# Performance work log

Hardware: AMD Instinct MI355X
Metric: run time of the kernel (lower is better)

Reference implementation:

```python
import jax, jax.numpy as jnp
import numpy as np

DIM = 512
DEPTH = 4
E = 2 ** DEPTH          # 16 experts
HID = 4 * DIM           # mult = 4
B, S = 8, 4096


def setup_inputs() -> dict:
    key = jax.random.key(0)
    ks = jax.random.split(key, 7)
    sc_in = 1.0 / np.sqrt(DIM)
    sc_hid = 1.0 / np.sqrt(HID)
    return {
        "x": jax.random.normal(ks[0], (B, S, DIM), jnp.float32),
        "Wr": jax.random.normal(ks[1], (E - 1, DIM), jnp.float32) * sc_in,
        "br": jax.random.normal(ks[2], (E - 1,), jnp.float32) * 0.01,
        "W1": jax.random.normal(ks[3], (E, DIM, HID), jnp.float32) * sc_in,
        "b1": jax.random.normal(ks[4], (E, HID), jnp.float32) * 0.01,
        "W2": jax.random.normal(ks[5], (E, HID, DIM), jnp.float32) * sc_hid,
        "b2": jax.random.normal(ks[6], (E, DIM), jnp.float32) * 0.01,
    }


def _fff_forward(x, Wr, br, W1, b1, W2, b2):
    Bb, Ss, D = x.shape
    E_ = W1.shape[0]
    depth = int(np.log2(E_))
    xf = x.reshape(-1, D)                      # [N, D]
    N = xf.shape[0]

    # Hard binary-tree routing (inference path of the torch module).
    leaf = jnp.zeros((N,), jnp.int32)
    for d in range(depth):
        off = 2 ** d - 1
        cnt = 2 ** d
        # logits for all routers at this tree level: [N, cnt]
        logits = xf @ Wr[off:off + cnt].T + br[off:off + cnt]
        sel = jnp.take_along_axis(logits, leaf[:, None], axis=1)[:, 0]
        leaf = leaf * 2 + (sel > 0).astype(jnp.int32)

    onehot = jax.nn.one_hot(leaf, E_, dtype=xf.dtype)  # [N, E]

    # Dense weighted-sum dispatch: scan over the (small, fixed) expert axis,
    # accumulating masked expert outputs. Peak extra memory is one [N, HID]
    # activation at a time.
    def body(acc, params):
        w1, bb1, w2, bb2, m = params            # m: [N]
        h = jax.nn.gelu(xf @ w1 + bb1, approximate=False)  # exact GELU (torch nn.GELU)
        y = h @ w2 + bb2
        return acc + m[:, None] * y, None

    out, _ = jax.lax.scan(body, jnp.zeros_like(xf), (W1, b1, W2, b2, onehot.T))
    return out.reshape(Bb, Ss, D)


def reference(x, Wr, br, W1, b1, W2, b2):
    return _fff_forward(x, Wr, br, W1, b1, W2, b2)
```

## Files before the change

kernel.cpp:

```cpp
#include <hip/hip_runtime.h>
#include <math.h>

#define NTOK   32768
#define DMODEL 512
#define HIDDEN 2048
#define NEXP   16
#define TM     128
#define TN     128
#define BK     64
#define MAXT   272
#define PADN   (MAXT * TM)
#define CPAD   16

typedef short bf16x8 __attribute__((ext_vector_type(8)));
typedef float f32x4  __attribute__((ext_vector_type(4)));

__device__ __forceinline__ short f2bf(float f) {
  union { float f; unsigned int u; } v; v.f = f;
  unsigned int r = v.u + 0x7FFFu + ((v.u >> 16) & 1u);
  return (short)(r >> 16);
}

__device__ __forceinline__ void gload_lds16(const void* g, void* l) {
  __builtin_amdgcn_global_load_lds(
      (const __attribute__((address_space(1))) void*)g,
      (__attribute__((address_space(3))) void*)l, 16, 0, 0);
}

__global__ void init_kernel(int* counts, int* cursors) {
  counts[threadIdx.x] = 0; cursors[threadIdx.x] = 0;
}

__global__ __launch_bounds__(256) void route_kernel(
    const float* __restrict__ x, const float* __restrict__ Wr,
    const float* __restrict__ br, short* __restrict__ xb,
    int* __restrict__ leafArr) {
  const int w = threadIdx.x >> 6, l = threadIdx.x & 63;
  const int tok = blockIdx.x * 4 + w;
  const float4* xr = (const float4*)(x + (size_t)tok * DMODEL);
  float4 a0 = xr[l * 2], a1 = xr[l * 2 + 1];

  union { bf16x8 v; short s[8]; } u;
  u.s[0] = f2bf(a0.x); u.s[1] = f2bf(a0.y); u.s[2] = f2bf(a0.z); u.s[3] = f2bf(a0.w);
  u.s[4] = f2bf(a1.x); u.s[5] = f2bf(a1.y); u.s[6] = f2bf(a1.z); u.s[7] = f2bf(a1.w);
  *((bf16x8*)(xb + (size_t)tok * DMODEL) + l) = u.v;

  int leaf = 0;
  for (int d = 0; d < 4; ++d) {
    const int node = (1 << d) - 1 + leaf;
    const float4* wr4 = (const float4*)(Wr + (size_t)node * DMODEL);
    float4 b0 = wr4[l * 2], b1v = wr4[l * 2 + 1];
    double s = (double)a0.x * (double)b0.x + (double)a0.y * (double)b0.y +
               (double)a0.z * (double)b0.z + (double)a0.w * (double)b0.w +
               (double)a1.x * (double)b1v.x + (double)a1.y * (double)b1v.y +
               (double)a1.z * (double)b1v.z + (double)a1.w * (double)b1v.w;
    for (int off = 32; off; off >>= 1) s += __shfl_xor(s, off);
    double sel = s + (double)br[node];
    leaf = leaf * 2 + (sel > 0.0 ? 1 : 0);
  }
  if (l == 0) leafArr[tok] = leaf;
}

__global__ __launch_bounds__(256) void count_kernel(
    const int* __restrict__ leafArr, int* __restrict__ counts,
    int* __restrict__ idx) {
  __shared__ int lcnt[NEXP];
  const int tid = threadIdx.x;
  if (tid < NEXP) lcnt[tid] = 0;
  __syncthreads();
  const int tok = blockIdx.x * 256 + tid;
  atomicAdd(&lcnt[leafArr[tok]], 1);
  __syncthreads();
  if (tid < NEXP && lcnt[tid]) atomicAdd(&counts[tid * CPAD], lcnt[tid]);
  for (int i = blockIdx.x * 256 + tid; i < PADN; i += gridDim.x * 256) idx[i] = 0;
}

__global__ void scan_kernel(const int* __restrict__ counts, int* poff, int* ntiles,
                            int* texp, int* tval) {
  if (threadIdx.x == 0) {
    int po = 0, nt = 0;
    for (int e = 0; e < NEXP; ++e) {
      poff[e] = po;
      const int c = counts[e * CPAD];
      const int t = (c + TM - 1) >> 7;
      for (int i = 0; i < t; ++i) {
        texp[nt] = e;
        int v = c - i * TM; if (v > TM) v = TM;
        tval[nt] = v;
        ++nt;
      }
      po += t << 7;
    }
    poff[NEXP] = po;
    *ntiles = nt;
  }
}

__global__ __launch_bounds__(256) void scatter_kernel(
    const int* __restrict__ leafArr, const int* __restrict__ poff,
    int* cursors, int* __restrict__ idx) {
  __shared__ int lcnt[NEXP], lbase[NEXP];
  const int tid = threadIdx.x;
  if (tid < NEXP) lcnt[tid] = 0;
  __syncthreads();
  const int tok = blockIdx.x * 256 + tid;
  const int e = leafArr[tok];
  const int r = atomicAdd(&lcnt[e], 1);
  __syncthreads();
  if (tid < NEXP) lbase[tid] = lcnt[tid] ? atomicAdd(&cursors[tid * CPAD], lcnt[tid]) : 0;
  __syncthreads();
  idx[poff[e] + lbase[e] + r] = tok;
}

__global__ void tconv_kernel(const float* __restrict__ src, short* __restrict__ dst,
                             int R, int C) {
  __shared__ float tile[32][33];
  const int tx = threadIdx.x, ty = threadIdx.y;
  const int c0 = blockIdx.x * 32, r0 = blockIdx.y * 32;
  const size_t eoff = (size_t)blockIdx.z * R * C;
  for (int i = 0; i < 4; ++i)
    tile[ty + i * 8][tx] = src[eoff + (size_t)(r0 + ty + i * 8) * C + c0 + tx];
  __syncthreads();
  for (int i = 0; i < 4; ++i)
    dst[eoff + (size_t)(c0 + ty + i * 8) * R + r0 + tx] = f2bf(tile[tx][ty + i * 8]);
}

__global__ __launch_bounds__(256) void gemm1_kernel(
    const short* __restrict__ Xb, const short* __restrict__ W1T,
    const float* __restrict__ b1, const int* __restrict__ idx,
    const int* __restrict__ texp, const int* __restrict__ ntiles,
    short* __restrict__ H, int g0) {
  const int lt = blockIdx.x;
  const int t = g0 + lt;
  if (t >= *ntiles) return;
  const int e = texp[t];
  const int c0 = blockIdx.y * TN;

  __shared__ short As[TM * BK];
  __shared__ short Bs[TN * BK];

  const int tid = threadIdx.x, w = tid >> 6, lane = tid & 63;
  const int q = lane >> 4, cc = lane & 15;
  const int wr = (w >> 1) * 64, wc = (w & 1) * 64;
  const int srow = lane >> 3, skk = (lane & 7) * 8;

  f32x4 acc[4][4];
  const f32x4 zero = {0.f, 0.f, 0.f, 0.f};
  for (int mi = 0; mi < 4; ++mi)
    for (int ni = 0; ni < 4; ++ni) acc[mi][ni] = zero;

  for (int k0 = 0; k0 < DMODEL; k0 += BK) {
    __syncthreads();
    for (int ii = 0; ii < 4; ++ii) {
      const int i = w * 4 + ii;
      const int trow = i * 8 + srow;
      const int gt = idx[t * TM + trow];
      gload_lds16(Xb + (size_t)gt * DMODEL + k0 + skk, As + i * 512);
      const int nn = c0 + i * 8 + srow;
      gload_lds16(W1T + ((size_t)e * HIDDEN + nn) * DMODEL + k0 + skk, Bs + i * 512);
    }
    __syncthreads();
    for (int ki = 0; ki < 2; ++ki) {
      const int kof = ki * 32 + q * 8;
      bf16x8 af[4], bfv[4];
      for (int mi = 0; mi < 4; ++mi)
        af[mi] = *(const bf16x8*)(As + (wr + mi * 16 + cc) * BK + kof);
      for (int ni = 0; ni < 4; ++ni)
        bfv[ni] = *(const bf16x8*)(Bs + (wc + ni * 16 + cc) * BK + kof);
      for (int mi = 0; mi < 4; ++mi)
        for (int ni = 0; ni < 4; ++ni)
          acc[mi][ni] = __builtin_amdgcn_mfma_f32_16x16x32_bf16(af[mi], bfv[ni], acc[mi][ni], 0, 0, 0);
    }
  }

  for (int ni = 0; ni < 4; ++ni) {
    const int col = c0 + wc + ni * 16 + cc;
    const float bv = b1[e * HIDDEN + col];
    for (int mi = 0; mi < 4; ++mi) {
      for (int r = 0; r < 4; ++r) {
        const int row = wr + mi * 16 + q * 4 + r;
        float v = acc[mi][ni][r] + bv;
        v = 0.5f * v * (1.0f + erff(v * 0.70710678118654752f));
        H[((size_t)lt * TM + row) * HIDDEN + col] = f2bf(v);
      }
    }
  }
}

__global__ __launch_bounds__(256) void gemm2_kernel(
    const short* __restrict__ H, const short* __restrict__ W2T,
    const float* __restrict__ b2, const int* __restrict__ idx,
    const int* __restrict__ texp, const int* __restrict__ tval,
    const int* __restrict__ ntiles, float* __restrict__ out, int g0) {
  const int lt = blockIdx.x;
  const int t = g0 + lt;
  if (t >= *ntiles) return;
  const int e = texp[t];
  const int c0 = blockIdx.y * TN;

  __shared__ short As[TM * BK];
  __shared__ short Bs[TN * BK];

  const int tid = threadIdx.x, w = tid >> 6, lane = tid & 63;
  const int q = lane >> 4, cc = lane & 15;
  const int wr = (w >> 1) * 64, wc = (w & 1) * 64;
  const int srow = lane >> 3, skk = (lane & 7) * 8;

  f32x4 acc[4][4];
  const f32x4 zero = {0.f, 0.f, 0.f, 0.f};
  for (int mi = 0; mi < 4; ++mi)
    for (int ni = 0; ni < 4; ++ni) acc[mi][ni] = zero;

  for (int k0 = 0; k0 < HIDDEN; k0 += BK) {
    __syncthreads();
    for (int ii = 0; ii < 4; ++ii) {
      const int i = w * 4 + ii;
      const int trow = i * 8 + srow;
      gload_lds16(H + ((size_t)lt * TM + trow) * HIDDEN + k0 + skk, As + i * 512);
      const int nn = c0 + i * 8 + srow;
      gload_lds16(W2T + ((size_t)e * DMODEL + nn) * HIDDEN + k0 + skk, Bs + i * 512);
    }
    __syncthreads();
    for (int ki = 0; ki < 2; ++ki) {
      const int kof = ki * 32 + q * 8;
      bf16x8 af[4], bfv[4];
      for (int mi = 0; mi < 4; ++mi)
        af[mi] = *(const bf16x8*)(As + (wr + mi * 16 + cc) * BK + kof);
      for (int ni = 0; ni < 4; ++ni)
        bfv[ni] = *(const bf16x8*)(Bs + (wc + ni * 16 + cc) * BK + kof);
      for (int mi = 0; mi < 4; ++mi)
        for (int ni = 0; ni < 4; ++ni)
          acc[mi][ni] = __builtin_amdgcn_mfma_f32_16x16x32_bf16(af[mi], bfv[ni], acc[mi][ni], 0, 0, 0);
    }
  }

  const int nv = tval[t];
  for (int ni = 0; ni < 4; ++ni) {
    const int col = c0 + wc + ni * 16 + cc;
    const float bv = b2[e * DMODEL + col];
    for (int mi = 0; mi < 4; ++mi) {
      for (int r = 0; r < 4; ++r) {
        const int row = wr + mi * 16 + q * 4 + r;
        if (row < nv) {
          const int tok = idx[t * TM + row];
          out[(size_t)tok * DMODEL + col] = acc[mi][ni][r] + bv;
        }
      }
    }
  }
}

extern "C" void kernel_launch(void* const* d_in, const int* in_sizes, int n_in,
                              void* d_out, int out_size, void* d_ws, size_t ws_size,
                              hipStream_t stream) {
  (void)in_sizes; (void)n_in; (void)out_size;
  const float* x  = (const float*)d_in[0];
  const float* Wr = (const float*)d_in[1];
  const float* br = (const float*)d_in[2];
  const float* W1 = (const float*)d_in[3];
  const float* b1 = (const float*)d_in[4];
  const float* W2 = (const float*)d_in[5];
  const float* b2 = (const float*)d_in[6];
  float* out = (float*)d_out;
  char* ws = (char*)d_ws;

  int* counts  = (int*)(ws + 0);
  int* cursors = (int*)(ws + 1024);
  int* poff    = (int*)(ws + 2048);
  int* ntiles  = (int*)(ws + 2304);
  int* texp    = (int*)(ws + 4096);
  int* tval    = (int*)(ws + 8192);
  int* leafA   = (int*)(ws + 16384);
  int* idx     = (int*)(ws + 16384 + 131072);

  const size_t MB32 = 33554432ull;
  short* Xb  = (short*)(ws + (1ull << 20));
  short* W1T = (short*)(ws + (1ull << 20) + MB32);
  short* W2T = (short*)(ws + (1ull << 20) + 2 * MB32);
  short* Hb  = (short*)(ws + (1ull << 20) + 3 * MB32);
  const size_t o_h = (1ull << 20) + 3 * MB32;
  const size_t perTile = (size_t)TM * HIDDEN * sizeof(short);

  int TPG = MAXT;
  if (ws_size < o_h + (size_t)MAXT * perTile) {
    size_t avail = ws_size > o_h ? ws_size - o_h : 0;
    TPG = (int)(avail / perTile);
    if (TPG < 1) TPG = 1;
  }
  const int ngroups = (MAXT + TPG - 1) / TPG;

  hipLaunchKernelGGL(init_kernel,    dim3(1),          dim3(256),   0, stream, counts, cursors);
  hipLaunchKernelGGL(route_kernel,   dim3(NTOK / 4),   dim3(256),   0, stream, x, Wr, br, Xb, leafA);
  hipLaunchKernelGGL(count_kernel,   dim3(NTOK / 256), dim3(256),   0, stream, leafA, counts, idx);
  hipLaunchKernelGGL(scan_kernel,    dim3(1),          dim3(64),    0, stream, counts, poff, ntiles, texp, tval);
  hipLaunchKernelGGL(scatter_kernel, dim3(NTOK / 256), dim3(256),   0, stream, leafA, poff, cursors, idx);
  hipLaunchKernelGGL(tconv_kernel,   dim3(64, 16, 16), dim3(32, 8), 0, stream, W1, W1T, DMODEL, HIDDEN);
  hipLaunchKernelGGL(tconv_kernel,   dim3(16, 64, 16), dim3(32, 8), 0, stream, W2, W2T, HIDDEN, DMODEL);

  for (int g = 0; g < ngroups; ++g) {
    hipLaunchKernelGGL(gemm1_kernel, dim3(TPG, HIDDEN / TN), dim3(256), 0, stream,
                       Xb, W1T, b1, idx, texp, ntiles, Hb, g * TPG);
    hipLaunchKernelGGL(gemm2_kernel, dim3(TPG, DMODEL / TN), dim3(256), 0, stream,
                       Hb, W2T, b2, idx, texp, tval, ntiles, out, g * TPG);
  }
}
```

Baseline: 659.0 us.

## Swizzle LDS tiles, stage GEMM1 epilogue through LDS, use tanh GELU

```diff
diff --git a/kernel.cpp b/kernel.cpp
--- a/kernel.cpp
+++ b/kernel.cpp
@@ -25,6 +25,15 @@
   __builtin_amdgcn_global_load_lds(
       (const __attribute__((address_space(1))) void*)g,
       (__attribute__((address_space(3))) void*)l, 16, 0, 0);
+}
+
+__device__ __forceinline__ float gelu_f(float v) {
+  const float u = v * (0.7978845608f + 0.0356774081f * v * v);
+  const float au = fabsf(u);
+  const float z = __expf(-2.0f * au);
+  float T = (1.0f - z) / (1.0f + z);
+  T = copysignf(T, u);
+  return 0.5f * v * (1.0f + T);
 }
 
 __global__ void init_kernel(int* counts, int* cursors) {
@@ -136,13 +145,15 @@
   const int e = texp[t];
   const int c0 = blockIdx.y * TN;
 
-  __shared__ short As[TM * BK];
-  __shared__ short Bs[TN * BK];
+  __shared__ short smem[TM * BK * 2];
+  short* As = smem;
+  short* Bs = smem + TM * BK;
 
   const int tid = threadIdx.x, w = tid >> 6, lane = tid & 63;
   const int q = lane >> 4, cc = lane & 15;
   const int wr = (w >> 1) * 64, wc = (w & 1) * 64;
-  const int srow = lane >> 3, skk = (lane & 7) * 8;
+  const int srow = lane >> 3;
+  const int sk = ((lane & 7) ^ srow) * 8;
 
   f32x4 acc[4][4];
   const f32x4 zero = {0.f, 0.f, 0.f, 0.f};
@@ -155,35 +166,46 @@
       const int i = w * 4 + ii;
       const int trow = i * 8 + srow;
       const int gt = idx[t * TM + trow];
-      gload_lds16(Xb + (size_t)gt * DMODEL + k0 + skk, As + i * 512);
+      gload_lds16(Xb + (size_t)gt * DMODEL + k0 + sk, As + i * 512);
       const int nn = c0 + i * 8 + srow;
-      gload_lds16(W1T + ((size_t)e * HIDDEN + nn) * DMODEL + k0 + skk, Bs + i * 512);
+      gload_lds16(W1T + ((size_t)e * HIDDEN + nn) * DMODEL + k0 + sk, Bs + i * 512);
     }
     __syncthreads();
     for (int ki = 0; ki < 2; ++ki) {
-      const int kof = ki * 32 + q * 8;
+      const int ch = ki * 4 + q;
+      const int sw = (ch ^ (cc & 7)) << 3;
       bf16x8 af[4], bfv[4];
       for (int mi = 0; mi < 4; ++mi)
-        af[mi] = *(const bf16x8*)(As + (wr + mi * 16 + cc) * BK + kof);
+        af[mi] = *(const bf16x8*)(As + (wr + mi * 16 + cc) * BK + sw);
       for (int ni = 0; ni < 4; ++ni)
-        bfv[ni] = *(const bf16x8*)(Bs + (wc + ni * 16 + cc) * BK + kof);
+        bfv[ni] = *(const bf16x8*)(Bs + (wc + ni * 16 + cc) * BK + sw);
       for (int mi = 0; mi < 4; ++mi)
         for (int ni = 0; ni < 4; ++ni)
           acc[mi][ni] = __builtin_amdgcn_mfma_f32_16x16x32_bf16(af[mi], bfv[ni], acc[mi][ni], 0, 0, 0);
     }
   }
 
+  __syncthreads();
+  short* Cs = smem;
   for (int ni = 0; ni < 4; ++ni) {
-    const int col = c0 + wc + ni * 16 + cc;
-    const float bv = b1[e * HIDDEN + col];
+    const int col = wc + ni * 16 + cc;
+    const float bv = b1[e * HIDDEN + c0 + col];
     for (int mi = 0; mi < 4; ++mi) {
       for (int r = 0; r < 4; ++r) {
         const int row = wr + mi * 16 + q * 4 + r;
-        float v = acc[mi][ni][r] + bv;
-        v = 0.5f * v * (1.0f + erff(v * 0.70710678118654752f));
-        H[((size_t)lt * TM + row) * HIDDEN + col] = f2bf(v);
+        const float v = gelu_f(acc[mi][ni][r] + bv);
+        Cs[row * 128 + ((((col >> 3) ^ (row & 15)) << 3) | (col & 7))] = f2bf(v);
       }
     }
+  }
+  __syncthreads();
+  for (int it = 0; it < 8; ++it) {
+    const int lin = tid + it * 256;
+    const int row = lin >> 4;
+    const int s = lin & 15;
+    const bf16x8 vv = *(const bf16x8*)(Cs + row * 128 + s * 8);
+    const int ch = s ^ (row & 15);
+    *(bf16x8*)(H + ((size_t)lt * TM + row) * HIDDEN + c0 + (ch << 3)) = vv;
   }
 }
 
@@ -198,13 +220,15 @@
   const int e = texp[t];
   const int c0 = blockIdx.y * TN;
 
-  __shared__ short As[TM * BK];
-  __shared__ short Bs[TN * BK];
+  __shared__ short smem[TM * BK * 2];
+  short* As = smem;
+  short* Bs = smem + TM * BK;
 
   const int tid = threadIdx.x, w = tid >> 6, lane = tid & 63;
   const int q = lane >> 4, cc = lane & 15;
   const int wr = (w >> 1) * 64, wc = (w & 1) * 64;
-  const int srow = lane >> 3, skk = (lane & 7) * 8;
+  const int srow = lane >> 3;
+  const int sk = ((lane & 7) ^ srow) * 8;
 
   f32x4 acc[4][4];
   const f32x4 zero = {0.f, 0.f, 0.f, 0.f};
@@ -216,18 +240,19 @@
     for (int ii = 0; ii < 4; ++ii) {
       const int i = w * 4 + ii;
       const int trow = i * 8 + srow;
-      gload_lds16(H + ((size_t)lt * TM + trow) * HIDDEN + k0 + skk, As + i * 512);
+      gload_lds16(H + ((size_t)lt * TM + trow) * HIDDEN + k0 + sk, As + i * 512);
       const int nn = c0 + i * 8 + srow;
-      gload_lds16(W2T + ((size_t)e * DMODEL + nn) * HIDDEN + k0 + skk, Bs + i * 512);
+      gload_lds16(W2T + ((size_t)e * DMODEL + nn) * HIDDEN + k0 + sk, Bs + i * 512);
     }
     __syncthreads();
     for (int ki = 0; ki < 2; ++ki) {
-      const int kof = ki * 32 + q * 8;
+      const int ch = ki * 4 + q;
+      const int sw = (ch ^ (cc & 7)) << 3;
       bf16x8 af[4], bfv[4];
       for (int mi = 0; mi < 4; ++mi)
-        af[mi] = *(const bf16x8*)(As + (wr + mi * 16 + cc) * BK + kof);
+        af[mi] = *(const bf16x8*)(As + (wr + mi * 16 + cc) * BK + sw);
       for (int ni = 0; ni < 4; ++ni)
-        bfv[ni] = *(const bf16x8*)(Bs + (wc + ni * 16 + cc) * BK + kof);
+        bfv[ni] = *(const bf16x8*)(Bs + (wc + ni * 16 + cc) * BK + sw);
       for (int mi = 0; mi < 4; ++mi)
         for (int ni = 0; ni < 4; ++ni)
           acc[mi][ni] = __builtin_amdgcn_mfma_f32_16x16x32_bf16(af[mi], bfv[ni], acc[mi][ni], 0, 0, 0);
```

Measured after the change: 582.5 us. 1.13x faster.
